# Performance work log

Hardware: AMD Instinct MI355X
Metric: run time of the kernel (lower is better)

Reference implementation:

```python
import jax, jax.numpy as jnp
import numpy as np

HIDDEN = 1024
N_HEADS = 16
HEAD_DIM = HIDDEN // N_HEADS  # 64; RoPE applied only to first HEAD_DIM channels (head 0)
NUM_BUCKETS = 32
MAX_DISTANCE = 128
MLP_HIDDEN = 4 * HIDDEN
B, N = 2, 2048


def _rotate_half(x):
    # interleaved pairs [a0,b0,a1,b1,...] -> [-b0,a0,-b1,a1,...]
    sh = x.shape
    xr = x.reshape(sh[:-1] + (sh[-1] // 2, 2))
    x1, x2 = xr[..., 0], xr[..., 1]
    return jnp.stack([-x2, x1], axis=-1).reshape(sh)


def _rel_bucket(n, num_buckets=NUM_BUCKETS, max_distance=MAX_DISTANCE):
    # bidirectional T5 bucketing
    ctx = jnp.arange(n)[:, None]
    mem = jnp.arange(n)[None, :]
    rp = mem - ctx  # [n, n]
    nb = num_buckets // 2
    buckets = jnp.where(rp > 0, nb, 0)
    rp = jnp.abs(rp)
    max_exact = nb // 2
    is_small = rp < max_exact
    log_ratio = jnp.log(jnp.maximum(rp, 1).astype(jnp.float32) / max_exact)
    rpl = max_exact + (log_ratio / np.log(max_distance / max_exact) * (nb - max_exact)).astype(jnp.int32)
    rpl = jnp.minimum(rpl, nb - 1)
    return buckets + jnp.where(is_small, rp, rpl)


def _ln(x, eps=1e-6):
    # LayerNorm without affine (DiT elementwise_affine=False)
    m = jnp.mean(x, axis=-1, keepdims=True)
    v = jnp.mean(jnp.square(x - m), axis=-1, keepdims=True)
    return (x - m) * jax.lax.rsqrt(v + eps)


def setup_inputs() -> dict:
    key = jax.random.key(0)
    ks = jax.random.split(key, 12)
    s = 0.02
    return {
        "x": jax.random.normal(ks[0], (B, N, HIDDEN), dtype=jnp.float32),
        "c": jax.random.normal(ks[1], (B, HIDDEN), dtype=jnp.float32),
        "w_ada": jax.random.normal(ks[2], (HIDDEN, 6 * HIDDEN), dtype=jnp.float32) * s,
        "b_ada": jnp.zeros((6 * HIDDEN,), dtype=jnp.float32),
        "w_qkv": jax.random.normal(ks[3], (HIDDEN, 3 * HIDDEN), dtype=jnp.float32) * s,
        "b_qkv": jnp.zeros((3 * HIDDEN,), dtype=jnp.float32),
        "w_out": jax.random.normal(ks[4], (HIDDEN, HIDDEN), dtype=jnp.float32) * s,
        "b_out": jnp.zeros((HIDDEN,), dtype=jnp.float32),
        "rel_table": jax.random.normal(ks[5], (NUM_BUCKETS, N_HEADS), dtype=jnp.float32) * s,
        "w_mlp1": jax.random.normal(ks[6], (HIDDEN, MLP_HIDDEN), dtype=jnp.float32) * s,
        "b_mlp1": jnp.zeros((MLP_HIDDEN,), dtype=jnp.float32),
        "w_mlp2": jax.random.normal(ks[7], (MLP_HIDDEN, HIDDEN), dtype=jnp.float32) * s,
        "b_mlp2": jnp.zeros((HIDDEN,), dtype=jnp.float32),
    }


def reference(x, c, w_ada, b_ada, w_qkv, b_qkv, w_out, b_out, rel_table,
              w_mlp1, b_mlp1, w_mlp2, b_mlp2):
    Bb, n, hid = x.shape
    hd = HEAD_DIM

    # AdaLN-Zero modulation params from conditioning
    mod = jax.nn.silu(c) @ w_ada + b_ada  # [B, 6*hid]
    sh_msa, sc_msa, g_msa, sh_mlp, sc_mlp, g_mlp = jnp.split(mod, 6, axis=-1)

    # --- attention branch ---
    h = _ln(x) * (1.0 + sc_msa[:, None, :]) + sh_msa[:, None, :]
    qkv = h @ w_qkv + b_qkv
    q, k, v = jnp.split(qkv, 3, axis=-1)  # each [B, N, hid]

    # partial RoPE: only first head_dim channels (head 0), interleaved-duplicated freqs
    t = jnp.arange(n, dtype=jnp.float32)
    inv_freq = 1.0 / (10000.0 ** (jnp.arange(0, hd, 2, dtype=jnp.float32) / hd))
    fr = t[:, None] * inv_freq[None, :]               # [N, hd/2]
    fr = jnp.stack([fr, fr], axis=-1).reshape(n, hd)  # [N, hd] interleaved dup
    cos, sin = jnp.cos(fr)[None], jnp.sin(fr)[None]

    def partial_rope(a):
        r, u = a[..., :hd], a[..., hd:]
        r = r * cos + _rotate_half(r) * sin
        return jnp.concatenate([r, u], axis=-1)

    q = partial_rope(q)
    k = partial_rope(k)

    qh = q.reshape(Bb, n, N_HEADS, hd)
    kh = k.reshape(Bb, n, N_HEADS, hd)
    vh = v.reshape(Bb, n, N_HEADS, hd)

    scores = jnp.einsum('bqhd,bkhd->bhqk', qh, kh) / np.float32(np.sqrt(hd))
    bias = rel_table[_rel_bucket(n)]                 # [N, N, H]
    scores = scores + jnp.transpose(bias, (2, 0, 1))[None]  # [1,H,N,N]
    attn = jax.nn.softmax(scores, axis=-1)
    ctxv = jnp.einsum('bhqk,bkhd->bqhd', attn, vh).reshape(Bb, n, hid)
    attn_out = ctxv @ w_out + b_out
    x = x + g_msa[:, None, :] * attn_out

    # --- MLP branch ---
    h2 = _ln(x) * (1.0 + sc_mlp[:, None, :]) + sh_mlp[:, None, :]
    m = jax.nn.gelu(h2 @ w_mlp1 + b_mlp1, approximate=True) @ w_mlp2 + b_mlp2
    return x + g_mlp[:, None, :] * m
```

## Files before the change

### kernel.cpp

```cpp
#include <hip/hip_runtime.h>
#include <hip/hip_bf16.h>

#define SEQ 2048

typedef float f32x4 __attribute__((ext_vector_type(4)));
typedef float f32x16 __attribute__((ext_vector_type(16)));
typedef short short8 __attribute__((ext_vector_type(8)));
typedef int int4v __attribute__((ext_vector_type(4)));

static __device__ __forceinline__ unsigned short f2bf(float f) {
  __hip_bfloat16 h = __float2bfloat16(f);
  unsigned short u;
  __builtin_memcpy(&u, &h, 2);
  return u;
}
static __device__ __forceinline__ float bf2f(unsigned short u) {
  __hip_bfloat16 h;
  __builtin_memcpy(&h, &u, 2);
  return __bfloat162float(h);
}
static __device__ __forceinline__ void gload16(const void* g, void* l) {
  __builtin_amdgcn_global_load_lds(
      (const __attribute__((address_space(1))) void*)g,
      (__attribute__((address_space(3))) void*)l, 16, 0, 0);
}
static __device__ __forceinline__ float gelu_t(float x) {
  float t = x * x;
  float z = x * fmaf(0.1029442695044937f, t, 2.3021181827964594f);
  return x * __builtin_amdgcn_rcpf(1.f + exp2f(-z));
}
static __device__ __forceinline__ unsigned int cvtpk(float lo, float hi) {
  unsigned int r;
  asm("v_cvt_pk_bf16_f32 %0, %1, %2" : "=v"(r) : "v"(lo), "v"(hi));
  return r;
}
static __device__ __forceinline__ void rope_pair(short8& v, int m, int i, float pos) {
  const float fr = exp2f(-(float)(2 * i) * (13.287712379549449f / 64.f));
  const float ang = pos * fr;
  const float sn = sinf(ang), cs = cosf(ang);
  const float x0 = bf2f((unsigned short)v[2 * m]);
  const float x1 = bf2f((unsigned short)v[2 * m + 1]);
  v[2 * m] = (short)f2bf(x0 * cs - x1 * sn);
  v[2 * m + 1] = (short)f2bf(x1 * cs + x0 * sn);
}


#define SOFTMAX_M0 16.0f
__global__ void prep_misc(const float* __restrict__ c, float* __restrict__ siluc,
                          const float* __restrict__ rel_table, float* __restrict__ brp) {
  const int bid = blockIdx.x, t = threadIdx.x;
  if (bid < 8) {
    int i = bid * 256 + t;
    float v = c[i];
    siluc[i] = v / (1.f + expf(-v));
  } else {
    int idx = (bid - 8) * 256 + t;
    int h = idx >> 12, pos = idx & 4095;
    int rp = pos - 2047;
    int bucket = rp > 0 ? 16 : 0;
    int a = rp < 0 ? -rp : rp;
    int bi;
    if (a < 8) {
      bi = a;
    } else {
      bi = 8 + (int)(logf((float)a / 8.f) / 2.772588722239781f * 8.f);
      if (bi > 15) bi = 15;
    }
    brp[idx] = rel_table[(bucket + bi) * 16 + h] * 1.4426950408889634f - SOFTMAX_M0;
  }
}

__global__ void mod_part_k(const float* __restrict__ siluc, const float* __restrict__ w_ada,
                           float* __restrict__ part) {
  int gid = blockIdx.x * 256 + threadIdx.x;
  int kc = gid / 12288;
  int idx = gid - kc * 12288;
  int b = idx / 6144;
  int j = idx - b * 6144;
  const float* cp = siluc + b * 1024 + kc * 64;
  const float* wp = w_ada + (size_t)kc * 64 * 6144 + j;
  float acc = 0.f;
#pragma unroll 8
  for (int k = 0; k < 64; ++k) acc += cp[k] * wp[(size_t)k * 6144];
  part[gid] = acc;
}

__global__ void mod_reduce_k(const float* __restrict__ part, const float* __restrict__ b_ada,
                             float* __restrict__ mod) {
  int idx = blockIdx.x * 256 + threadIdx.x;
  int j = idx % 6144;
  float a = b_ada[j];
#pragma unroll
  for (int kc = 0; kc < 16; ++kc) a += part[kc * 12288 + idx];
  mod[idx] = a;
}

__global__ void transpose_all(const float* __restrict__ w_qkv, const float* __restrict__ w_out,
                              const float* __restrict__ w_mlp1, const float* __restrict__ w_mlp2,
                              unsigned short* __restrict__ dq, unsigned short* __restrict__ dwo,
                              unsigned short* __restrict__ dm1, unsigned short* __restrict__ dm2) {
  __shared__ float tile[32][33];
  const int bid = blockIdx.x;
  const float* src;
  unsigned short* dst;
  int K, N, NT, r;
  if (bid < 3072) {
    src = w_qkv; dst = dq; K = 1024; N = 3072; NT = 96; r = bid;
  } else if (bid < 4096) {
    src = w_out; dst = dwo; K = 1024; N = 1024; NT = 32; r = bid - 3072;
  } else if (bid < 8192) {
    src = w_mlp1; dst = dm1; K = 1024; N = 4096; NT = 128; r = bid - 4096;
  } else {
    src = w_mlp2; dst = dm2; K = 4096; N = 1024; NT = 32; r = bid - 8192;
  }
  const int nt = r % NT, kt = r / NT;
  const int t = threadIdx.x;
  const int col = t & 31, r0 = t >> 5;
#pragma unroll
  for (int i = 0; i < 4; ++i) {
    int rr = r0 + i * 8;
    tile[rr][col] = src[(size_t)(kt * 32 + rr) * N + nt * 32 + col];
  }
  __syncthreads();
#pragma unroll
  for (int i = 0; i < 4; ++i) {
    int rr = r0 + i * 8;
    dst[(size_t)(nt * 32 + rr) * K + kt * 32 + col] = f2bf(tile[col][rr]);
  }
}

__global__ void ln_mod(const float* __restrict__ x, const float* __restrict__ mod,
                       unsigned short* __restrict__ out, int sh_off, int sc_off) {
  int row = blockIdx.x;
  int b = row >> 11;
  int t = threadIdx.x;
  const float4 v = ((const float4*)(x + (size_t)row * 1024))[t];
  float s1 = v.x + v.y + v.z + v.w;
  float s2 = v.x * v.x + v.y * v.y + v.z * v.z + v.w * v.w;
#pragma unroll
  for (int off = 32; off; off >>= 1) {
    s1 += __shfl_xor(s1, off);
    s2 += __shfl_xor(s2, off);
  }
  __shared__ float red[8];
  int w = t >> 6, lane = t & 63;
  if (lane == 0) { red[w] = s1; red[4 + w] = s2; }
  __syncthreads();
  s1 = red[0] + red[1] + red[2] + red[3];
  s2 = red[4] + red[5] + red[6] + red[7];
  float mean = s1 * (1.f / 1024.f);
  float var = s2 * (1.f / 1024.f) - mean * mean;
  float rstd = rsqrtf(var + 1e-6f);
  const float* mb = mod + (size_t)b * 6144;
  int col = t * 4;
  ushort4 o4;
  o4.x = f2bf((v.x - mean) * rstd * (1.f + mb[sc_off + col + 0]) + mb[sh_off + col + 0]);
  o4.y = f2bf((v.y - mean) * rstd * (1.f + mb[sc_off + col + 1]) + mb[sh_off + col + 1]);
  o4.z = f2bf((v.z - mean) * rstd * (1.f + mb[sc_off + col + 2]) + mb[sh_off + col + 2]);
  o4.w = f2bf((v.w - mean) * rstd * (1.f + mb[sc_off + col + 3]) + mb[sh_off + col + 3]);
  *((ushort4*)(out + (size_t)row * 1024 + col)) = o4;
}

__global__ void kvpack(const unsigned short* __restrict__ qkv, unsigned short* __restrict__ kpk,
                       unsigned short* __restrict__ vpk) {
  const int kt = blockIdx.x;
  const int bh = blockIdx.y;
  const int b = bh >> 4, h = bh & 15;
  const int t = threadIdx.x;
  const int s = t >> 6, lane = t & 63;
  const int l31 = lane & 31, hi = lane >> 5;
  const size_t outbase = ((size_t)(bh * 64 + kt) * 4 + s) * 512 + lane * 8;
  {
    const unsigned short* src =
        qkv + (size_t)(b * SEQ + kt * 32 + l31) * 3072 + 1024 + h * 64 + s * 16 + hi * 8;
    short8 kv = *(const short8*)src;
    if (h == 0) {
      const float pos = (float)(kt * 32 + l31);
      const int d0 = s * 16 + hi * 8;
#pragma unroll
      for (int m = 0; m < 4; ++m) rope_pair(kv, m, (d0 >> 1) + m, pos);
    }
    *(short8*)(kpk + outbase) = kv;
  }
  {
    const int krow = kt * 32 + (s & 1) * 16 + hi * 8;
    const int d = (s >> 1) * 32 + l31;
    const unsigned short* src = qkv + (size_t)(b * SEQ + krow) * 3072 + 2048 + h * 64 + d;
    unsigned short v[8];
#pragma unroll
    for (int j = 0; j < 8; ++j) v[j] = src[(size_t)j * 3072];
    *(short8*)(vpk + outbase) = *(const short8*)v;
  }
}

template <int MODE, int BM, int BN, int PIPE>
__global__ __launch_bounds__(256) void gemm_bt(
    const unsigned short* __restrict__ A, const unsigned short* __restrict__ Bt,
    const float* __restrict__ bias, void* __restrict__ outp, const float* __restrict__ res,
    const float* __restrict__ mod, int goff, int N, int K) {
  constexpr int NBUF = PIPE ? 2 : 1;
  __shared__ __align__(16) unsigned short a_lds[NBUF][BM * 64];
  __shared__ __align__(16) unsigned short b_lds[NBUF][BN * 64];
  constexpr int WM = BM / 2, WN = BN / 2;
  constexpr int MT = WM / 16, NT = WN / 16;
  const int t = threadIdx.x;
  const int lane = t & 63;
  const int l15 = lane & 15, l4 = lane >> 4;
  const int w = t >> 6;
  const int wr = w >> 1, wc = w & 1;
  const int gx = gridDim.x;
  const int nwg = gx * gridDim.y;
  int wg = blockIdx.y * gx + blockIdx.x;
  wg = (wg & 7) * (nwg >> 3) + (wg >> 3);
  const int by = wg / gx, bx = wg - by * gx;
  const int rowA0 = by * BM;
  const int rowB0 = bx * BN;
  const int wub = t & ~63;

  f32x4 acc[MT][NT];
#pragma unroll
  for (int m = 0; m < MT; ++m)
#pragma unroll
    for (int n = 0; n < NT; ++n) acc[m][n] = (f32x4){0.f, 0.f, 0.f, 0.f};

  auto stage = [&](int buf, int kt) {
#pragma unroll
    for (int rnd = 0; rnd < BM / 32; ++rnd) {
      const int idx = rnd * 256 + t;
      const int row = idx >> 3;
      const int cb = ((idx & 7) << 4) ^ ((row & 7) << 4);
      const char* sa = (const char*)(A + (size_t)(rowA0 + row) * K + kt) + cb;
      gload16(sa, (char*)(&a_lds[buf][0]) + (size_t)(rnd * 256 + wub) * 16);
    }
#pragma unroll
    for (int rnd = 0; rnd < BN / 32; ++rnd) {
      const int idx = rnd * 256 + t;
      const int row = idx >> 3;
      const int cb = ((idx & 7) << 4) ^ ((row & 7) << 4);
      const char* sb = (const char*)(Bt + (size_t)(rowB0 + row) * K + kt) + cb;
      gload16(sb, (char*)(&b_lds[buf][0]) + (size_t)(rnd * 256 + wub) * 16);
    }
  };

  auto compute = [&](int buf) {
#pragma unroll
    for (int kb = 0; kb < 2; ++kb) {
      short8 af[MT], bfr[NT];
#pragma unroll
      for (int m = 0; m < MT; ++m) {
        int row = wr * WM + m * 16 + l15;
        int cb = (kb * 64 + l4 * 16) ^ ((row & 7) << 4);
        af[m] = *(const short8*)((const char*)(&a_lds[buf][0]) + row * 128 + cb);
      }
#pragma unroll
      for (int n = 0; n < NT; ++n) {
        int row = wc * WN + n * 16 + l15;
        int cb = (kb * 64 + l4 * 16) ^ ((row & 7) << 4);
        bfr[n] = *(const short8*)((const char*)(&b_lds[buf][0]) + row * 128 + cb);
      }
      __builtin_amdgcn_s_setprio(1);
#pragma unroll
      for (int m = 0; m < MT; ++m)
#pragma unroll
        for (int n = 0; n < NT; ++n)
          acc[m][n] = __builtin_amdgcn_mfma_f32_16x16x32_bf16(af[m], bfr[n], acc[m][n], 0, 0, 0);
      __builtin_amdgcn_s_setprio(0);
    }
  };

  if (PIPE) {
    stage(0, 0);
    __syncthreads();
    int cur = 0;
    for (int kt = 0; kt < K; kt += 64) {
      if (kt + 64 < K) stage(cur ^ 1, kt + 64);
      compute(cur);
      __syncthreads();
      cur ^= 1;
    }
  } else {
    for (int kt = 0; kt < K; kt += 64) {
      stage(0, kt);
      __syncthreads();
      compute(0);
      __syncthreads();
    }
  }

#pragma unroll
  for (int n = 0; n < NT; ++n) {
    const int col = rowB0 + wc * WN + n * 16 + l15;
    const float bv = bias[col];
#pragma unroll
    for (int m = 0; m < MT; ++m) {
      const int row0 = rowA0 + wr * WM + m * 16 + l4 * 4;
#pragma unroll
      for (int r = 0; r < 4; ++r) {
        float v = acc[m][n][r] + bv;
        const size_t o = (size_t)(row0 + r) * N + col;
        if (MODE == 0) {
          ((unsigned short*)outp)[o] = f2bf(v);
        } else if (MODE == 1) {
          ((unsigned short*)outp)[o] = f2bf(gelu_t(v));
        } else {
          float g = mod[(size_t)((row0 + r) >> 11) * 6144 + goff + col];
          ((float*)outp)[o] = res[o] + g * v;
        }
      }
    }
  }
}

__global__ __launch_bounds__(256) void attn_k(const unsigned short* __restrict__ qkv,
                                              const unsigned short* __restrict__ kpk,
                                              const unsigned short* __restrict__ vpk,
                                              const float* __restrict__ brp_all,
                                              unsigned short* __restrict__ op0,
                                              unsigned short* __restrict__ op1,
                                              float* __restrict__ lpart) {
  const int t = threadIdx.x;
  const int w = t >> 6;
  const int lane = t & 63;
  const int l31 = lane & 31;
  const int hi = lane >> 5;
  const int wg = blockIdx.x;
  const int xcd = wg & 7, idx = wg >> 3;
  const int bh = xcd * 4 + (idx >> 5);
  const int rem = idx & 31;
  const int qt = rem >> 1, ks = rem & 1;
  const int b = bh >> 4, h = bh & 15;
  const int qw = qt * 128 + w * 32;
  const float SC = 0.125f * 1.4426950408889634f;
  const float* brp = brp_all + (size_t)h * 4096;

  short8 qfr[4];
  {
    const unsigned short* qrow = qkv + (size_t)(b * SEQ + qw + l31) * 3072 + h * 64 + hi * 8;
#pragma unroll
    for (int kk = 0; kk < 4; ++kk) qfr[kk] = *(const short8*)(qrow + kk * 16);
    if (h == 0) {
      const float pos = (float)(qw + l31);
#pragma unroll
      for (int kk = 0; kk < 4; ++kk) {
        const int d0 = kk * 16 + hi * 8;
#pragma unroll
        for (int m = 0; m < 4; ++m) rope_pair(qfr[kk], m, (d0 >> 1) + m, pos);
      }
    }
  }
  const float bfar_pos = brp[4095], bfar_neg = brp[0];
  const float* bql = brp + 2047 + 4 * hi - (qw + l31);

  short8 ones;
#pragma unroll
  for (int i = 0; i < 8; ++i) ones[i] = (short)0x3F80;

  const unsigned short* kp = kpk + ((size_t)(bh * 64 + ks * 16)) * 2048 + lane * 8;
  const unsigned short* vp = vpk + ((size_t)(bh * 64 + ks * 16)) * 2048 + lane * 8;

  short8 kfrA[4], vfrA[4], kfrB[4], vfrB[4];
#pragma unroll
  for (int s = 0; s < 4; ++s) {
    kfrA[s] = *(const short8*)(kp + s * 512);
    vfrA[s] = *(const short8*)(vp + s * 512);
  }
  kp += 2048;
  vp += 2048;

  f32x16 oacc0 = {}, oacc1 = {}, lacc = {};
  int kbase = ks * 512;

#define ATTN_TILE(KF, VF, KFN, VFN)                                                       \
  do {                                                                                    \
    KFN[0] = *(const short8*)(kp);                                                        \
    KFN[1] = *(const short8*)(kp + 512);                                                  \
    KFN[2] = *(const short8*)(kp + 1024);                                                 \
    KFN[3] = *(const short8*)(kp + 1536);                                                 \
    VFN[0] = *(const short8*)(vp);                                                        \
    VFN[1] = *(const short8*)(vp + 512);                                                  \
    VFN[2] = *(const short8*)(vp + 1024);                                                 \
    VFN[3] = *(const short8*)(vp + 1536);                                                 \
    kp += 2048;                                                                           \
    vp += 2048;                                                                           \
    f32x16 sacc = {};                                                                     \
    sacc = __builtin_amdgcn_mfma_f32_32x32x16_bf16(KF[0], qfr[0], sacc, 0, 0, 0);         \
    sacc = __builtin_amdgcn_mfma_f32_32x32x16_bf16(KF[1], qfr[1], sacc, 0, 0, 0);         \
    sacc = __builtin_amdgcn_mfma_f32_32x32x16_bf16(KF[2], qfr[2], sacc, 0, 0, 0);         \
    sacc = __builtin_amdgcn_mfma_f32_32x32x16_bf16(KF[3], qfr[3], sacc, 0, 0, 0);         \
    float p[16];                                                                          \
    const int dd = kbase - qw;                                                            \
    if (dd >= 128 || dd <= -128) {                                                        \
      const float bf_ = (dd > 0) ? bfar_pos : bfar_neg;                                   \
      _Pragma("unroll") for (int r = 0; r < 16; ++r)                                      \
          p[r] = __builtin_amdgcn_exp2f(fmaf(sacc[r], SC, bf_));                          \
    } else {                                                                              \
      const float* bp = bql + kbase;                                                      \
      _Pragma("unroll") for (int r = 0; r < 16; ++r)                                      \
          p[r] = __builtin_amdgcn_exp2f(fmaf(sacc[r], SC, bp[(r & 3) + 8 * (r >> 2)]));   \
    }                                                                                     \
    unsigned int x0 = cvtpk(p[0], p[1]), x1 = cvtpk(p[2], p[3]);                          \
    unsigned int y0 = cvtpk(p[4], p[5]), y1 = cvtpk(p[6], p[7]);                          \
    asm("v_permlane32_swap_b32 %0, %1" : "+v"(x0), "+v"(y0));                             \
    asm("v_permlane32_swap_b32 %0, %1" : "+v"(x1), "+v"(y1));                             \
    unsigned int x2 = cvtpk(p[8], p[9]), x3 = cvtpk(p[10], p[11]);                        \
    unsigned int y2 = cvtpk(p[12], p[13]), y3 = cvtpk(p[14], p[15]);                      \
    asm("v_permlane32_swap_b32 %0, %1" : "+v"(x2), "+v"(y2));                             \
    asm("v_permlane32_swap_b32 %0, %1" : "+v"(x3), "+v"(y3));                             \
    int4v pi0 = {(int)x0, (int)x1, (int)y0, (int)y1};                                     \
    int4v pi1 = {(int)x2, (int)x3, (int)y2, (int)y3};                                     \
    short8 pf0 = __builtin_bit_cast(short8, pi0);                                         \
    short8 pf1 = __builtin_bit_cast(short8, pi1);                                         \
    lacc = __builtin_amdgcn_mfma_f32_32x32x16_bf16(ones, pf0, lacc, 0, 0, 0);             \
    lacc = __builtin_amdgcn_mfma_f32_32x32x16_bf16(ones, pf1, lacc, 0, 0, 0);             \
    oacc0 = __builtin_amdgcn_mfma_f32_32x32x16_bf16(VF[0], pf0, oacc0, 0, 0, 0);          \
    oacc0 = __builtin_amdgcn_mfma_f32_32x32x16_bf16(VF[1], pf1, oacc0, 0, 0, 0);          \
    oacc1 = __builtin_amdgcn_mfma_f32_32x32x16_bf16(VF[2], pf0, oacc1, 0, 0, 0);          \
    oacc1 = __builtin_amdgcn_mfma_f32_32x32x16_bf16(VF[3], pf1, oacc1, 0, 0, 0);          \
    kbase += 32;                                                                          \
  } while (0)

#pragma unroll 1
  for (int it = 0; it < 8; ++it) {
    ATTN_TILE(kfrA, vfrA, kfrB, vfrB);
    ATTN_TILE(kfrB, vfrB, kfrA, vfrA);
  }
#undef ATTN_TILE

  unsigned short* op = ks ? op1 : op0;
  unsigned short* orow = op + (size_t)(b * SEQ + qw + l31) * 1024 + h * 64;
#pragma unroll
  for (int r = 0; r < 16; r += 2) {
    const int d = (r & 3) + 8 * (r >> 2) + 4 * hi;
    *(unsigned int*)(orow + d) = cvtpk(oacc0[r], oacc0[r + 1]);
    *(unsigned int*)(orow + 32 + d) = cvtpk(oacc1[r], oacc1[r + 1]);
  }
  if (lane < 32) lpart[(size_t)ks * 65536 + (size_t)(b * SEQ + qw + l31) * 16 + h] = lacc[0];
}

__global__ void attn_combine(const unsigned short* __restrict__ op0,
                             const unsigned short* __restrict__ op1,
                             const float* __restrict__ lpart,
                             unsigned short* __restrict__ ctxv) {
  const int row = blockIdx.x;
  const int t = threadIdx.x;
  const int h = t >> 4;
  const size_t base = (size_t)row * 1024 + t * 4;
  ushort4 a = *(const ushort4*)(op0 + base);
  ushort4 c = *(const ushort4*)(op1 + base);
  const float l = lpart[(size_t)row * 16 + h] + lpart[65536 + (size_t)row * 16 + h];
  const float inv = 1.f / l;
  ushort4 o;
  o.x = f2bf((bf2f(a.x) + bf2f(c.x)) * inv);
  o.y = f2bf((bf2f(a.y) + bf2f(c.y)) * inv);
  o.z = f2bf((bf2f(a.z) + bf2f(c.z)) * inv);
  o.w = f2bf((bf2f(a.w) + bf2f(c.w)) * inv);
  *(ushort4*)(ctxv + base) = o;
}

extern "C" void kernel_launch(void* const* d_in, const int* in_sizes, int n_in, void* d_out,
                              int out_size, void* d_ws, size_t ws_size, hipStream_t stream) {
  (void)in_sizes; (void)n_in; (void)out_size; (void)ws_size;
  const float* x = (const float*)d_in[0];
  const float* c = (const float*)d_in[1];
  const float* w_ada = (const float*)d_in[2];
  const float* b_ada = (const float*)d_in[3];
  const float* w_qkv = (const float*)d_in[4];
  const float* b_qkv = (const float*)d_in[5];
  const float* w_out = (const float*)d_in[6];
  const float* b_out = (const float*)d_in[7];
  const float* rel_t = (const float*)d_in[8];
  const float* w_mlp1 = (const float*)d_in[9];
  const float* b_mlp1 = (const float*)d_in[10];
  const float* w_mlp2 = (const float*)d_in[11];
  const float* b_mlp2 = (const float*)d_in[12];
  float* out = (float*)d_out;
  char* ws = (char*)d_ws;

  constexpr size_t OFF_WQKVT = 0;
  constexpr size_t OFF_WOUTT = OFF_WQKVT + (size_t)3072 * 1024 * 2;
  constexpr size_t OFF_WM1T = OFF_WOUTT + (size_t)1024 * 1024 * 2;
  constexpr size_t OFF_WM2T = OFF_WM1T + (size_t)4096 * 1024 * 2;
  constexpr size_t OFF_H = OFF_WM2T + (size_t)1024 * 4096 * 2;
  constexpr size_t OFF_QKV = OFF_H + (size_t)4096 * 1024 * 2;
  constexpr size_t OFF_VT = OFF_QKV + (size_t)4096 * 3072 * 2;
  constexpr size_t OFF_CTXV = OFF_VT + (size_t)32 * 64 * 2048 * 2;
  constexpr size_t OFF_MID = OFF_CTXV + (size_t)4096 * 1024 * 2;
  constexpr size_t OFF_SILU = OFF_MID + (size_t)4096 * 4096 * 2;
  constexpr size_t OFF_MOD = OFF_SILU + 2048 * 4;
  constexpr size_t OFF_BRP = OFF_MOD + 12288 * 4;
  constexpr size_t OFF_PART = OFF_BRP + 65536 * 4;
  constexpr size_t OFF_OPART0 = OFF_H;
  constexpr size_t OFF_OPART1 = OFF_MID + (size_t)16 * 1024 * 1024;
  constexpr size_t OFF_LPART = OFF_PART;

  unsigned short* wqkvT = (unsigned short*)(ws + OFF_WQKVT);
  unsigned short* woutT = (unsigned short*)(ws + OFF_WOUTT);
  unsigned short* wm1T = (unsigned short*)(ws + OFF_WM1T);
  unsigned short* wm2T = (unsigned short*)(ws + OFF_WM2T);
  unsigned short* hbuf = (unsigned short*)(ws + OFF_H);
  unsigned short* qkvbuf = (unsigned short*)(ws + OFF_QKV);
  unsigned short* vpkbuf = (unsigned short*)(ws + OFF_VT);
  unsigned short* ctxvbuf = (unsigned short*)(ws + OFF_CTXV);
  unsigned short* midbuf = (unsigned short*)(ws + OFF_MID);
  unsigned short* kpkbuf = (unsigned short*)(ws + OFF_MID);
  float* siluc = (float*)(ws + OFF_SILU);
  float* modb = (float*)(ws + OFF_MOD);
  float* brp = (float*)(ws + OFF_BRP);
  float* part = (float*)(ws + OFF_PART);
  unsigned short* op0 = (unsigned short*)(ws + OFF_OPART0);
  unsigned short* op1 = (unsigned short*)(ws + OFF_OPART1);
  float* lpart = (float*)(ws + OFF_LPART);

  prep_misc<<<264, 256, 0, stream>>>(c, siluc, rel_t, brp);
  mod_part_k<<<768, 256, 0, stream>>>(siluc, w_ada, part);
  mod_reduce_k<<<48, 256, 0, stream>>>(part, b_ada, modb);
  transpose_all<<<12288, 256, 0, stream>>>(w_qkv, w_out, w_mlp1, w_mlp2, wqkvT, woutT, wm1T,
                                           wm2T);

  ln_mod<<<4096, 256, 0, stream>>>(x, modb, hbuf, 0, 1024);
  gemm_bt<0, 128, 128, 0><<<dim3(24, 32), 256, 0, stream>>>(hbuf, wqkvT, b_qkv, qkvbuf, nullptr,
                                                            nullptr, 0, 3072, 1024);
  kvpack<<<dim3(64, 32), 256, 0, stream>>>(qkvbuf, kpkbuf, vpkbuf);
  attn_k<<<1024, 256, 0, stream>>>(qkvbuf, kpkbuf, vpkbuf, brp, op0, op1, lpart);
  attn_combine<<<4096, 256, 0, stream>>>(op0, op1, lpart, ctxvbuf);
  gemm_bt<2, 64, 64, 1><<<dim3(16, 64), 256, 0, stream>>>(ctxvbuf, woutT, b_out, out, x, modb,
                                                          2048, 1024, 1024);
  ln_mod<<<4096, 256, 0, stream>>>(out, modb, hbuf, 3072, 4096);
  gemm_bt<1, 128, 128, 0><<<dim3(32, 32), 256, 0, stream>>>(hbuf, wm1T, b_mlp1, midbuf, nullptr,
                                                            nullptr, 0, 4096, 1024);
  gemm_bt<2, 64, 64, 1><<<dim3(16, 64), 256, 0, stream>>>(midbuf, wm2T, b_mlp2, out, out, modb,
                                                          5120, 1024, 4096);
}
```

Measured before the change: 242.8 us.

## Pre-pack out/MLP2 weights in MFMA fragment order and load B directly to registers

```diff
diff --git a/kernel.cpp b/kernel.cpp
--- a/kernel.cpp
+++ b/kernel.cpp
@@ -103,15 +103,15 @@
   const int bid = blockIdx.x;
   const float* src;
   unsigned short* dst;
-  int K, N, NT, r;
+  int K, N, NT, r, packed;
   if (bid < 3072) {
-    src = w_qkv; dst = dq; K = 1024; N = 3072; NT = 96; r = bid;
+    src = w_qkv; dst = dq; K = 1024; N = 3072; NT = 96; r = bid; packed = 0;
   } else if (bid < 4096) {
-    src = w_out; dst = dwo; K = 1024; N = 1024; NT = 32; r = bid - 3072;
+    src = w_out; dst = dwo; K = 1024; N = 1024; NT = 32; r = bid - 3072; packed = 1;
   } else if (bid < 8192) {
-    src = w_mlp1; dst = dm1; K = 1024; N = 4096; NT = 128; r = bid - 4096;
+    src = w_mlp1; dst = dm1; K = 1024; N = 4096; NT = 128; r = bid - 4096; packed = 0;
   } else {
-    src = w_mlp2; dst = dm2; K = 4096; N = 1024; NT = 32; r = bid - 8192;
+    src = w_mlp2; dst = dm2; K = 4096; N = 1024; NT = 32; r = bid - 8192; packed = 1;
   }
   const int nt = r % NT, kt = r / NT;
   const int t = threadIdx.x;
@@ -125,7 +125,17 @@
 #pragma unroll
   for (int i = 0; i < 4; ++i) {
     int rr = r0 + i * 8;
-    dst[(size_t)(nt * 32 + rr) * K + kt * 32 + col] = f2bf(tile[col][rr]);
+    const int ocol = nt * 32 + rr;
+    const int ok = kt * 32 + col;
+    size_t off;
+    if (packed) {
+      const int bx = ocol >> 6, f = (ocol >> 4) & 3, lo15 = ocol & 15;
+      const int ks = ok >> 6, kb = (ok >> 5) & 1, lo4 = (ok >> 3) & 3, j = ok & 7;
+      off = ((((size_t)bx * (K >> 6) + ks) * 2 + kb) * 4 + f) * 512 + (lo4 * 16 + lo15) * 8 + j;
+    } else {
+      off = (size_t)ocol * K + ok;
+    }
+    dst[off] = f2bf(tile[col][rr]);
   }
 }
 
@@ -193,14 +203,14 @@
   }
 }
 
-template <int MODE, int BM, int BN, int PIPE>
+template <int MODE, int BM, int BN, int PIPE, int BP>
 __global__ __launch_bounds__(256) void gemm_bt(
     const unsigned short* __restrict__ A, const unsigned short* __restrict__ Bt,
     const float* __restrict__ bias, void* __restrict__ outp, const float* __restrict__ res,
     const float* __restrict__ mod, int goff, int N, int K) {
   constexpr int NBUF = PIPE ? 2 : 1;
   __shared__ __align__(16) unsigned short a_lds[NBUF][BM * 64];
-  __shared__ __align__(16) unsigned short b_lds[NBUF][BN * 64];
+  __shared__ __align__(16) unsigned short b_lds[NBUF][BP ? 64 : BN * 64];
   constexpr int WM = BM / 2, WN = BN / 2;
   constexpr int MT = WM / 16, NT = WN / 16;
   const int t = threadIdx.x;
@@ -217,6 +227,9 @@
   const int rowB0 = bx * BN;
   const int wub = t & ~63;
 
+  const unsigned short* bpk =
+      BP ? (Bt + ((size_t)bx * (K >> 6)) * 4096 + (size_t)(wc * 2) * 512 + lane * 8) : nullptr;
+
   f32x4 acc[MT][NT];
 #pragma unroll
   for (int m = 0; m < MT; ++m)
@@ -232,31 +245,37 @@
       const char* sa = (const char*)(A + (size_t)(rowA0 + row) * K + kt) + cb;
       gload16(sa, (char*)(&a_lds[buf][0]) + (size_t)(rnd * 256 + wub) * 16);
     }
-#pragma unroll
-    for (int rnd = 0; rnd < BN / 32; ++rnd) {
-      const int idx = rnd * 256 + t;
-      const int row = idx >> 3;
-      const int cb = ((idx & 7) << 4) ^ ((row & 7) << 4);
-      const char* sb = (const char*)(Bt + (size_t)(rowB0 + row) * K + kt) + cb;
-      gload16(sb, (char*)(&b_lds[buf][0]) + (size_t)(rnd * 256 + wub) * 16);
+    if (!BP) {
+#pragma unroll
+      for (int rnd = 0; rnd < BN / 32; ++rnd) {
+        const int idx = rnd * 256 + t;
+        const int row = idx >> 3;
+        const int cb = ((idx & 7) << 4) ^ ((row & 7) << 4);
+        const char* sb = (const char*)(Bt + (size_t)(rowB0 + row) * K + kt) + cb;
+        gload16(sb, (char*)(&b_lds[buf][0]) + (size_t)(rnd * 256 + wub) * 16);
+      }
     }
   };
 
-  auto compute = [&](int buf) {
+  auto compute = [&](int buf, int ks) {
 #pragma unroll
     for (int kb = 0; kb < 2; ++kb) {
       short8 af[MT], bfr[NT];
+#pragma unroll
+      for (int n = 0; n < NT; ++n) {
+        if (BP) {
+          bfr[n] = *(const short8*)(bpk + ((size_t)ks * 4096 + kb * 2048 + n * 512));
+        } else {
+          int row = wc * WN + n * 16 + l15;
+          int cb = (kb * 64 + l4 * 16) ^ ((row & 7) << 4);
+          bfr[n] = *(const short8*)((const char*)(&b_lds[buf][0]) + row * 128 + cb);
+        }
+      }
 #pragma unroll
       for (int m = 0; m < MT; ++m) {
         int row = wr * WM + m * 16 + l15;
         int cb = (kb * 64 + l4 * 16) ^ ((row & 7) << 4);
         af[m] = *(const short8*)((const char*)(&a_lds[buf][0]) + row * 128 + cb);
-      }
-#pragma unroll
-      for (int n = 0; n < NT; ++n) {
-        int row = wc * WN + n * 16 + l15;
-        int cb = (kb * 64 + l4 * 16) ^ ((row & 7) << 4);
-        bfr[n] = *(const short8*)((const char*)(&b_lds[buf][0]) + row * 128 + cb);
       }
       __builtin_amdgcn_s_setprio(1);
 #pragma unroll
@@ -274,7 +293,7 @@
     int cur = 0;
     for (int kt = 0; kt < K; kt += 64) {
       if (kt + 64 < K) stage(cur ^ 1, kt + 64);
-      compute(cur);
+      compute(cur, kt >> 6);
       __syncthreads();
       cur ^= 1;
     }
@@ -282,7 +301,7 @@
     for (int kt = 0; kt < K; kt += 64) {
       stage(0, kt);
       __syncthreads();
-      compute(0);
+      compute(0, kt >> 6);
       __syncthreads();
     }
   }
@@ -518,16 +537,16 @@
                                            wm2T);
 
   ln_mod<<<4096, 256, 0, stream>>>(x, modb, hbuf, 0, 1024);
-  gemm_bt<0, 128, 128, 0><<<dim3(24, 32), 256, 0, stream>>>(hbuf, wqkvT, b_qkv, qkvbuf, nullptr,
-                                                            nullptr, 0, 3072, 1024);
+  gemm_bt<0, 128, 128, 0, 0><<<dim3(24, 32), 256, 0, stream>>>(hbuf, wqkvT, b_qkv, qkvbuf,
+                                                               nullptr, nullptr, 0, 3072, 1024);
   kvpack<<<dim3(64, 32), 256, 0, stream>>>(qkvbuf, kpkbuf, vpkbuf);
   attn_k<<<1024, 256, 0, stream>>>(qkvbuf, kpkbuf, vpkbuf, brp, op0, op1, lpart);
   attn_combine<<<4096, 256, 0, stream>>>(op0, op1, lpart, ctxvbuf);
-  gemm_bt<2, 64, 64, 1><<<dim3(16, 64), 256, 0, stream>>>(ctxvbuf, woutT, b_out, out, x, modb,
-                                                          2048, 1024, 1024);
+  gemm_bt<2, 64, 64, 1, 1><<<dim3(16, 64), 256, 0, stream>>>(ctxvbuf, woutT, b_out, out, x, modb,
+                                                             2048, 1024, 1024);
   ln_mod<<<4096, 256, 0, stream>>>(out, modb, hbuf, 3072, 4096);
-  gemm_bt<1, 128, 128, 0><<<dim3(32, 32), 256, 0, stream>>>(hbuf, wm1T, b_mlp1, midbuf, nullptr,
-                                                            nullptr, 0, 4096, 1024);
-  gemm_bt<2, 64, 64, 1><<<dim3(16, 64), 256, 0, stream>>>(midbuf, wm2T, b_mlp2, out, out, modb,
-                                                          5120, 1024, 4096);
-}
+  gemm_bt<1, 128, 128, 0, 0><<<dim3(32, 32), 256, 0, stream>>>(hbuf, wm1T, b_mlp1, midbuf,
+                                                               nullptr, nullptr, 0, 4096, 1024);
+  gemm_bt<2, 64, 64, 1, 1><<<dim3(16, 64), 256, 0, stream>>>(midbuf, wm2T, b_mlp2, out, out,
+                                                             modb, 5120, 1024, 4096);
+}
```

After: 260.3 us. +7.2%, slower.
